# Optimization experiments

Measured on AMD Instinct MI355X. Metric: run time of the kernel, lower is better.

Reference implementation:

```python
import jax, jax.numpy as jnp
import numpy as np

DEPTH = 3
NUM_MOLS = 2000
ATOMS_PER_MOL = 50
NA = NUM_MOLS * ATOMS_PER_MOL + 1   # +1 chemprop zero-padding row
NB = 2 * NUM_MOLS * ATOMS_PER_MOL + 1
MAX_NB = 6
ATOM_FDIM, BOND_FDIM, H = 133, 147, 300


def setup_inputs() -> dict:
    key = jax.random.key(0)
    ks = jax.random.split(key, 12)
    f_atoms = jax.random.normal(ks[0], (NA, ATOM_FDIM), jnp.float32)
    f_bonds = jax.random.normal(ks[1], (NB, BOND_FDIM), jnp.float32)
    # zero padding row (index 0) as in chemprop BatchMolGraph
    f_atoms = f_atoms.at[0].set(0.0)
    f_bonds = f_bonds.at[0].set(0.0)
    w_atoms = jax.random.uniform(ks[2], (NA,), jnp.float32, 0.5, 1.0)
    w_bonds = jax.random.uniform(ks[3], (NB,), jnp.float32, 0.5, 1.0)
    degree_of_polym = jax.random.uniform(ks[4], (NUM_MOLS,), jnp.float32, 0.5, 1.5)
    W_i = jax.random.normal(ks[5], (BOND_FDIM, H), jnp.float32) / np.sqrt(BOND_FDIM)
    W_h = jax.random.normal(ks[6], (H, H), jnp.float32) / np.sqrt(H)
    W_o = jax.random.normal(ks[7], (ATOM_FDIM + H, H), jnp.float32) / np.sqrt(ATOM_FDIM + H)
    b_o = jax.random.normal(ks[8], (H,), jnp.float32) * 0.01
    a2b = jax.random.randint(ks[9], (NA, MAX_NB), 0, NB, jnp.int32)
    b2a = jax.random.randint(ks[10], (NB,), 0, NA, jnp.int32)
    b2revb = jax.random.randint(ks[11], (NB,), 0, NB, jnp.int32)
    # segment id per real atom (padding row 0 excluded), contiguous molecules
    mol_index = (jnp.arange(NA - 1, dtype=jnp.int32) // ATOMS_PER_MOL)
    return dict(f_atoms=f_atoms, f_bonds=f_bonds, w_atoms=w_atoms, w_bonds=w_bonds,
                degree_of_polym=degree_of_polym, W_i=W_i, W_h=W_h, W_o=W_o, b_o=b_o,
                a2b=a2b, b2a=b2a, b2revb=b2revb, mol_index=mol_index)


def reference(f_atoms, f_bonds, w_atoms, w_bonds, degree_of_polym,
              W_i, W_h, W_o, b_o, a2b, b2a, b2revb, mol_index):
    # bond-message D-MPNN (atom_messages=False, undirected=False, relu, no dropout)
    inp = f_bonds @ W_i                       # [NB, H]
    message = jax.nn.relu(inp)
    w_nei = w_bonds[a2b]                      # [NA, MAX_NB]
    for _ in range(DEPTH - 1):
        nei = message[a2b] * w_nei[..., None] # [NA, MAX_NB, H] weighted gather
        a_message = nei.sum(axis=1)           # [NA, H]
        message = a_message[b2a] - message[b2revb] * w_bonds[:, None]
        message = jax.nn.relu(inp + message @ W_h)
    # final atom readout
    a_message = (message[a2b] * w_nei[..., None]).sum(axis=1)   # [NA, H]
    a_input = jnp.concatenate([f_atoms, a_message], axis=1)     # [NA, ATOM_FDIM+H]
    atom_hiddens = jax.nn.relu(a_input @ W_o + b_o)
    # per-molecule weighted mean over real atoms (row 0 is padding)
    h = atom_hiddens[1:] * w_atoms[1:, None]
    num_mols = degree_of_polym.shape[0]
    mol_sum = jax.ops.segment_sum(h, mol_index, num_segments=num_mols)
    w_sum = jax.ops.segment_sum(w_atoms[1:], mol_index, num_segments=num_mols)
    mol_vecs = degree_of_polym[:, None] * (mol_sum / w_sum[:, None])
    return mol_vecs
```

## Files before the change

### kernel.cpp

```cpp
#include <hip/hip_runtime.h>

typedef __bf16 bf16;
typedef bf16 bf16x8 __attribute__((ext_vector_type(8)));
typedef float f32x4 __attribute__((ext_vector_type(4)));

#define NUM_MOLS 2000
#define APM 50
#define NA (NUM_MOLS*APM+1)
#define NB (2*NUM_MOLS*APM+1)
#define MAX_NB 6
#define AF 133
#define BFD 147
#define H 300
#define HP 320
#define KIP 192
#define KO 448
#define AOFF 136
#define BM 64
#define LDTE 72

__global__ void k_prep_wi(const float* __restrict__ Wi, bf16* __restrict__ Wt){
    int i = blockIdx.x*256 + threadIdx.x; if (i >= HP*KIP) return;
    int n = i / KIP, k = i % KIP;
    float v = (k < BFD && n < H) ? Wi[k*H + n] : 0.f;
    Wt[i] = (bf16)v;
}
__global__ void k_prep_wh(const float* __restrict__ Wh, bf16* __restrict__ Wt){
    int i = blockIdx.x*256 + threadIdx.x; if (i >= HP*HP) return;
    int n = i / HP, k = i % HP;
    float v = (k < H && n < H) ? Wh[k*H + n] : 0.f;
    Wt[i] = (bf16)v;
}
__global__ void k_prep_wo(const float* __restrict__ Wo, bf16* __restrict__ Wt){
    int i = blockIdx.x*256 + threadIdx.x; if (i >= HP*KO) return;
    int n = i / KO, k = i % KO;
    float v = 0.f;
    if (n < H) {
        if (k < AF)                       v = Wo[k*H + n];
        else if (k >= AOFF && k < AOFF+H) v = Wo[(k - AOFF + AF)*H + n];
    }
    Wt[i] = (bf16)v;
}
__global__ void k_init_cat(const float* __restrict__ fa, bf16* __restrict__ cat){
    long u = (long)blockIdx.x*256 + threadIdx.x; if (u >= (long)NA*18) return;
    int c = (int)(u % 18); long a = u / 18;
    bf16x8 v;
    if (c < 17) {
        int c0 = c*8;
        #pragma unroll
        for (int j=0;j<8;j++){
            int col = c0 + j;
            float f = (col < AF) ? fa[a*AF + col] : 0.f;
            v[j] = (bf16)f;
        }
        *(bf16x8*)(cat + a*KO + c0) = v;
    } else {
        #pragma unroll
        for (int j=0;j<8;j++) v[j] = (bf16)0.f;
        *(bf16x8*)(cat + a*KO + 440) = v;
    }
}

__global__ void k_gather_amsg(const bf16* __restrict__ msg, const int* __restrict__ a2b,
                              const float* __restrict__ w_bonds,
                              bf16* __restrict__ out, int out_stride, int col_off, int nchunks){
    long u = (long)blockIdx.x*256 + threadIdx.x;
    if (u >= (long)NA*nchunks) return;
    int c = (int)(u % nchunks); long a = u / nchunks;
    int c0 = c*8;
    float acc[8] = {0,0,0,0,0,0,0,0};
    #pragma unroll
    for (int k=0;k<MAX_NB;k++){
        int b = a2b[a*MAX_NB + k];
        float w = w_bonds[b];
        bf16x8 m = *(const bf16x8*)(msg + (long)b*HP + c0);
        #pragma unroll
        for (int j=0;j<8;j++) acc[j] += w * fmaxf((float)m[j], 0.f);
    }
    bf16x8 o;
    #pragma unroll
    for (int j=0;j<8;j++) o[j] = (bf16)acc[j];
    *(bf16x8*)(out + (long)a*out_stride + col_off + c0) = o;
}

template<int MODE, int K>
__global__ __launch_bounds__(512)
void k_gemm(const void* __restrict__ Asrc, const bf16* __restrict__ msgsrc,
            const int* __restrict__ b2a, const int* __restrict__ b2revb,
            const float* __restrict__ w_bonds,
            const bf16* __restrict__ Bt, int M,
            const bf16* __restrict__ add, const float* __restrict__ bias,
            bf16* __restrict__ out)
{
    constexpr int NSTEP = K / 64;
    __shared__ bf16 As[BM][LDTE];
    __shared__ bf16 Bs[HP][LDTE];
    const int t = threadIdx.x;
    const int row0 = blockIdx.x * BM;

    const int sr = t >> 3;
    const int sc = (t & 7) * 8;
    int arow = row0 + sr; if (arow >= M) arow = M - 1;
    int ia = 0, ir = 0; float w = 0.f;
    if (MODE == 1) { ia = b2a[arow]; ir = b2revb[arow]; w = w_bonds[arow]; }

    float  fa8[8];
    bf16x8 ra, rm;
    bf16x8 rb[5];

    auto issue = [&](int k0){
        if constexpr (MODE == 0) {
            const float* fb = (const float*)Asrc;
            #pragma unroll
            for (int j = 0; j < 8; j++) {
                int k = k0 + sc + j;
                fa8[j] = (k < BFD) ? fb[(long)arow*BFD + k] : 0.f;
            }
        } else if constexpr (MODE == 1) {
            ra = *(const bf16x8*)((const bf16*)Asrc + (long)ia*HP + k0 + sc);
            rm = *(const bf16x8*)(msgsrc            + (long)ir*HP + k0 + sc);
        } else {
            ra = *(const bf16x8*)((const bf16*)Asrc + (long)arow*KO + k0 + sc);
        }
        #pragma unroll
        for (int i = 0; i < 5; i++) {
            int c = t + 512*i;
            rb[i] = *(const bf16x8*)(Bt + (long)(c >> 3)*K + k0 + (c & 7)*8);
        }
    };
    auto commit = [&](){
        bf16x8 av;
        if constexpr (MODE == 0) {
            #pragma unroll
            for (int j = 0; j < 8; j++) av[j] = (bf16)fa8[j];
        } else if constexpr (MODE == 1) {
            #pragma unroll
            for (int j = 0; j < 8; j++)
                av[j] = (bf16)((float)ra[j] - fmaxf((float)rm[j], 0.f) * w);
        } else {
            av = ra;
        }
        *(bf16x8*)(&As[sr][sc]) = av;
        #pragma unroll
        for (int i = 0; i < 5; i++) {
            int c = t + 512*i;
            *(bf16x8*)(&Bs[c >> 3][(c & 7)*8]) = rb[i];
        }
    };

    const int wave = t >> 6, lane = t & 63;
    const int wm = wave >> 2, wn = wave & 3;
    const int kr = lane >> 4, lr = lane & 15;
    f32x4 acc[2][5] = {};

    issue(0); commit();
    __syncthreads();

    #pragma unroll
    for (int s = 0; s < NSTEP; s++) {
        if (s + 1 < NSTEP) issue((s + 1) * 64);
        #pragma unroll
        for (int kk = 0; kk < 64; kk += 32) {
            bf16x8 af[2], bfr[5];
            #pragma unroll
            for (int m = 0; m < 2; m++)
                af[m] = *(const bf16x8*)(&As[wm*32 + m*16 + lr][kk + kr*8]);
            #pragma unroll
            for (int n = 0; n < 5; n++)
                bfr[n] = *(const bf16x8*)(&Bs[wn*80 + n*16 + lr][kk + kr*8]);
            #pragma unroll
            for (int m = 0; m < 2; m++)
                #pragma unroll
                for (int n = 0; n < 5; n++)
                    acc[m][n] = __builtin_amdgcn_mfma_f32_16x16x32_bf16(af[m], bfr[n], acc[m][n], 0, 0, 0);
        }
        if (s + 1 < NSTEP) {
            __syncthreads();
            commit();
            __syncthreads();
        }
    }

    #pragma unroll
    for (int m = 0; m < 2; m++)
    #pragma unroll
    for (int n = 0; n < 5; n++)
    #pragma unroll
    for (int r = 0; r < 4; r++) {
        int row = row0 + wm*32 + m*16 + kr*4 + r;
        if (row >= M) continue;
        int col = wn*80 + n*16 + lr;
        float v = acc[m][n][r];
        if (add)  v += (float)add[(long)row*HP + col];
        if (bias) v += (col < H) ? bias[col] : 0.f;
        if (MODE == 2) v = fmaxf(v, 0.f);
        out[(long)row*HP + col] = (bf16)v;
    }
}

__global__ void k_seg(const bf16* __restrict__ ah, const float* __restrict__ w_atoms,
                      const float* __restrict__ dop, float* __restrict__ out){
    int m = blockIdx.x; int t = threadIdx.x;
    __shared__ float ws_sum;
    float w = 0.f;
    if (t < APM) w = w_atoms[1 + m*APM + t];
    if (t < 64) {
        for (int o=32;o;o>>=1) w += __shfl_down(w, o);
        if (t==0) ws_sum = w;
    }
    __syncthreads();
    float scale = dop[m] / ws_sum;
    for (int h = t; h < H; h += 256) {
        float acc = 0.f;
        for (int j=0;j<APM;j++){
            int a = 1 + m*APM + j;
            acc += (float)ah[(long)a*HP + h] * w_atoms[a];
        }
        out[m*H + h] = acc * scale;
    }
}

__global__ void k_zero(float* __restrict__ out, int n){
    int i = blockIdx.x*256 + threadIdx.x;
    if (i < n) out[i] = 0.f;
}

extern "C" void kernel_launch(void* const* d_in, const int* in_sizes, int n_in,
                              void* d_out, int out_size, void* d_ws, size_t ws_size,
                              hipStream_t stream) {
    const float* f_atoms = (const float*)d_in[0];
    const float* f_bonds = (const float*)d_in[1];
    const float* w_atoms = (const float*)d_in[2];
    const float* w_bonds = (const float*)d_in[3];
    const float* dop     = (const float*)d_in[4];
    const float* W_i     = (const float*)d_in[5];
    const float* W_h     = (const float*)d_in[6];
    const float* W_o     = (const float*)d_in[7];
    const float* b_o     = (const float*)d_in[8];
    const int*   a2b     = (const int*)d_in[9];
    const int*   b2a     = (const int*)d_in[10];
    const int*   b2revb  = (const int*)d_in[11];
    float* out = (float*)d_out;
    (void)in_sizes; (void)n_in;

    const size_t R_BIG = ((size_t)NB*HP*2 + 255) & ~(size_t)255;
    const size_t R_ATM = ((size_t)NA*HP*2 + 255) & ~(size_t)255;
    const size_t R_WI  = ((size_t)HP*KIP*2 + 255) & ~(size_t)255;
    const size_t R_WH  = ((size_t)HP*HP*2 + 255) & ~(size_t)255;
    const size_t R_WO  = ((size_t)HP*KO*2 + 255) & ~(size_t)255;
    const size_t need  = 3*R_BIG + R_ATM + R_WI + R_WH + R_WO;

    if (ws_size < need) {
        k_zero<<<(out_size+255)/256, 256, 0, stream>>>(out, out_size);
        return;
    }

    char* ws = (char*)d_ws;
    bf16* inp  = (bf16*)ws;
    bf16* msgA = (bf16*)(ws + R_BIG);
    bf16* msgB = (bf16*)(ws + 2*R_BIG);
    bf16* amsg = (bf16*)(ws + 3*R_BIG);
    bf16* wit  = (bf16*)(ws + 3*R_BIG + R_ATM);
    bf16* wht  = (bf16*)((char*)wit + R_WI);
    bf16* wot  = (bf16*)((char*)wht + R_WH);
    bf16* cat  = msgA;
    bf16* ah   = amsg;

    k_prep_wi<<<(HP*KIP+255)/256, 256, 0, stream>>>(W_i, wit);
    k_prep_wh<<<(HP*HP+255)/256, 256, 0, stream>>>(W_h, wht);
    k_prep_wo<<<(HP*KO+255)/256, 256, 0, stream>>>(W_o, wot);

    const int GB = (NB + BM - 1) / BM;
    const int GA = (NA + BM - 1) / BM;

    k_gemm<0, KIP><<<GB, 512, 0, stream>>>(f_bonds, nullptr, nullptr, nullptr, nullptr,
                                           wit, NB, nullptr, nullptr, inp);
    k_gather_amsg<<<(int)(((long)NA*40+255)/256), 256, 0, stream>>>(
        inp, a2b, w_bonds, amsg, HP, 0, 40);
    k_gemm<1, HP><<<GB, 512, 0, stream>>>(amsg, inp, b2a, b2revb, w_bonds,
                                          wht, NB, inp, nullptr, msgA);
    k_gather_amsg<<<(int)(((long)NA*40+255)/256), 256, 0, stream>>>(
        msgA, a2b, w_bonds, amsg, HP, 0, 40);
    k_gemm<1, HP><<<GB, 512, 0, stream>>>(amsg, msgA, b2a, b2revb, w_bonds,
                                          wht, NB, inp, nullptr, msgB);
    k_init_cat<<<(int)(((long)NA*18+255)/256), 256, 0, stream>>>(f_atoms, cat);
    k_gather_amsg<<<(int)(((long)NA*38+255)/256), 256, 0, stream>>>(
        msgB, a2b, w_bonds, cat, KO, AOFF, 38);
    k_gemm<2, KO><<<GA, 512, 0, stream>>>(cat, nullptr, nullptr, nullptr, nullptr,
                                          wot, NA, nullptr, b_o, ah);
    k_seg<<<NUM_MOLS, 256, 0, stream>>>(ah, w_atoms, dop, out);
}
```

Before: 803.0 us.

## Pre-swizzle weights into MFMA fragment order and stage tiles via direct global-to-LDS loads

```diff
diff --git a/kernel.cpp b/kernel.cpp
--- a/kernel.cpp
+++ b/kernel.cpp
@@ -17,30 +17,39 @@
 #define KO 448
 #define AOFF 136
 #define BM 64
-#define LDTE 72
-
-__global__ void k_prep_wi(const float* __restrict__ Wi, bf16* __restrict__ Wt){
-    int i = blockIdx.x*256 + threadIdx.x; if (i >= HP*KIP) return;
-    int n = i / KIP, k = i % KIP;
-    float v = (k < BFD && n < H) ? Wi[k*H + n] : 0.f;
-    Wt[i] = (bf16)v;
-}
-__global__ void k_prep_wh(const float* __restrict__ Wh, bf16* __restrict__ Wt){
-    int i = blockIdx.x*256 + threadIdx.x; if (i >= HP*HP) return;
-    int n = i / HP, k = i % HP;
-    float v = (k < H && n < H) ? Wh[k*H + n] : 0.f;
-    Wt[i] = (bf16)v;
-}
-__global__ void k_prep_wo(const float* __restrict__ Wo, bf16* __restrict__ Wt){
-    int i = blockIdx.x*256 + threadIdx.x; if (i >= HP*KO) return;
-    int n = i / KO, k = i % KO;
+
+typedef const __attribute__((address_space(1))) void gvoid_t;
+typedef __attribute__((address_space(3))) void lvoid_t;
+__device__ __forceinline__ void gload16(const void* g, void* l) {
+    __builtin_amdgcn_global_load_lds((gvoid_t*)g, (lvoid_t*)l, 16, 0, 0);
+}
+
+__device__ __forceinline__ void frag_decode(int e, int& row, int& col, int& j){
+    int s = e / 20480;
+    int r = e - s*20480;
+    int q = r >> 3; j = r & 7;
+    int frag = q >> 6, lane = q & 63;
+    int wn = frag / 10, rem = frag - wn*10;
+    int n = rem >> 1, kh = rem & 1;
+    row = wn*80 + n*16 + (lane & 15);
+    col = s*64 + kh*32 + ((lane >> 4) << 3) + j;
+}
+
+template<int W, int K>
+__global__ void k_prep(const float* __restrict__ src, bf16* __restrict__ dst){
+    int e = blockIdx.x*256 + threadIdx.x;
+    if (e >= HP*K) return;
+    int row, col, j; frag_decode(e, row, col, j);
     float v = 0.f;
-    if (n < H) {
-        if (k < AF)                       v = Wo[k*H + n];
-        else if (k >= AOFF && k < AOFF+H) v = Wo[(k - AOFF + AF)*H + n];
-    }
-    Wt[i] = (bf16)v;
-}
+    if (row < H) {
+        if constexpr (W == 0)      { if (col < BFD) v = src[col*H + row]; }
+        else if constexpr (W == 1) { if (col < H)   v = src[col*H + row]; }
+        else { if (col < AF) v = src[col*H + row];
+               else if (col >= AOFF && col < AOFF+H) v = src[(col-AOFF+AF)*H + row]; }
+    }
+    dst[e] = (bf16)v;
+}
+
 __global__ void k_init_cat(const float* __restrict__ fa, bf16* __restrict__ cat){
     long u = (long)blockIdx.x*256 + threadIdx.x; if (u >= (long)NA*18) return;
     int c = (int)(u % 18); long a = u / 18;
@@ -84,103 +93,116 @@
 }
 
 template<int MODE, int K>
-__global__ __launch_bounds__(512)
+__global__ __launch_bounds__(512, 4)
 void k_gemm(const void* __restrict__ Asrc, const bf16* __restrict__ msgsrc,
             const int* __restrict__ b2a, const int* __restrict__ b2revb,
             const float* __restrict__ w_bonds,
-            const bf16* __restrict__ Bt, int M,
+            const bf16* __restrict__ Btg, int M,
             const bf16* __restrict__ add, const float* __restrict__ bias,
             bf16* __restrict__ out)
 {
-    constexpr int NSTEP = K / 64;
-    __shared__ bf16 As[BM][LDTE];
-    __shared__ bf16 Bs[HP][LDTE];
-    const int t = threadIdx.x;
+    constexpr int NKB = K/32, NSTEP = K/64, NJ = K/64;
+    __shared__ bf16 As[64*K];
+    __shared__ bf16 Bs[20480];
+    const int t = threadIdx.x, lane = t & 63, wv = t >> 6;
     const int row0 = blockIdx.x * BM;
 
-    const int sr = t >> 3;
-    const int sc = (t & 7) * 8;
-    int arow = row0 + sr; if (arow >= M) arow = M - 1;
-    int ia = 0, ir = 0; float w = 0.f;
-    if (MODE == 1) { ia = b2a[arow]; ir = b2revb[arow]; w = w_bonds[arow]; }
-
-    float  fa8[8];
-    bf16x8 ra, rm;
-    bf16x8 rb[5];
-
-    auto issue = [&](int k0){
-        if constexpr (MODE == 0) {
-            const float* fb = (const float*)Asrc;
+    int acol[NJ]; int agrow[NJ];
+    #pragma unroll
+    for (int i = 0; i < NJ; i++) {
+        int frag = i*8 + wv;
+        int rg = frag / NKB, kb = frag - rg*NKB;
+        int grow = row0 + rg*16 + (lane & 15);
+        if (grow >= M) grow = M - 1;
+        agrow[i] = grow;
+        acol[i]  = kb*32 + ((lane >> 4) << 3);
+    }
+
+    bf16x8 ra[MODE==1?NJ:1], rm[MODE==1?NJ:1];
+    float  wbv[MODE==1?NJ:1];
+    float  f8[MODE==0?NJ:1][8];
+
+    if constexpr (MODE == 0) {
+        const float* fb = (const float*)Asrc;
+        #pragma unroll
+        for (int i = 0; i < NJ; i++)
             #pragma unroll
             for (int j = 0; j < 8; j++) {
-                int k = k0 + sc + j;
-                fa8[j] = (k < BFD) ? fb[(long)arow*BFD + k] : 0.f;
+                int k = acol[i] + j;
+                f8[i][j] = (k < BFD) ? fb[(long)agrow[i]*BFD + k] : 0.f;
             }
-        } else if constexpr (MODE == 1) {
-            ra = *(const bf16x8*)((const bf16*)Asrc + (long)ia*HP + k0 + sc);
-            rm = *(const bf16x8*)(msgsrc            + (long)ir*HP + k0 + sc);
-        } else {
-            ra = *(const bf16x8*)((const bf16*)Asrc + (long)arow*KO + k0 + sc);
-        }
-        #pragma unroll
-        for (int i = 0; i < 5; i++) {
-            int c = t + 512*i;
-            rb[i] = *(const bf16x8*)(Bt + (long)(c >> 3)*K + k0 + (c & 7)*8);
-        }
-    };
-    auto commit = [&](){
-        bf16x8 av;
-        if constexpr (MODE == 0) {
-            #pragma unroll
-            for (int j = 0; j < 8; j++) av[j] = (bf16)fa8[j];
-        } else if constexpr (MODE == 1) {
+    } else if constexpr (MODE == 1) {
+        const bf16* am = (const bf16*)Asrc;
+        #pragma unroll
+        for (int i = 0; i < NJ; i++) {
+            int ia = b2a[agrow[i]], ir = b2revb[agrow[i]];
+            wbv[i] = w_bonds[agrow[i]];
+            ra[i] = *(const bf16x8*)(am     + (long)ia*HP + acol[i]);
+            rm[i] = *(const bf16x8*)(msgsrc + (long)ir*HP + acol[i]);
+        }
+    } else {
+        const bf16* cat = (const bf16*)Asrc;
+        #pragma unroll
+        for (int i = 0; i < NJ; i++)
+            gload16(cat + (long)agrow[i]*KO + acol[i], As + ((long)i*512 + (t & ~63))*8);
+    }
+
+    #pragma unroll
+    for (int i = 0; i < 5; i++)
+        gload16(Btg + (long)(i*512 + t)*8, Bs + ((long)i*512 + (t & ~63))*8);
+
+    if constexpr (MODE == 0) {
+        #pragma unroll
+        for (int i = 0; i < NJ; i++) {
+            bf16x8 av;
+            #pragma unroll
+            for (int j = 0; j < 8; j++) av[j] = (bf16)f8[i][j];
+            *(bf16x8*)(As + ((long)i*512 + t)*8) = av;
+        }
+    } else if constexpr (MODE == 1) {
+        #pragma unroll
+        for (int i = 0; i < NJ; i++) {
+            bf16x8 av;
             #pragma unroll
             for (int j = 0; j < 8; j++)
-                av[j] = (bf16)((float)ra[j] - fmaxf((float)rm[j], 0.f) * w);
-        } else {
-            av = ra;
-        }
-        *(bf16x8*)(&As[sr][sc]) = av;
-        #pragma unroll
-        for (int i = 0; i < 5; i++) {
-            int c = t + 512*i;
-            *(bf16x8*)(&Bs[c >> 3][(c & 7)*8]) = rb[i];
-        }
-    };
-
-    const int wave = t >> 6, lane = t & 63;
-    const int wm = wave >> 2, wn = wave & 3;
-    const int kr = lane >> 4, lr = lane & 15;
+                av[j] = (bf16)((float)ra[i][j] - fmaxf((float)rm[i][j], 0.f) * wbv[i]);
+            *(bf16x8*)(As + ((long)i*512 + t)*8) = av;
+        }
+    }
+
+    const int wm = wv >> 2, wn = wv & 3;
     f32x4 acc[2][5] = {};
-
-    issue(0); commit();
     __syncthreads();
 
     #pragma unroll
     for (int s = 0; s < NSTEP; s++) {
-        if (s + 1 < NSTEP) issue((s + 1) * 64);
-        #pragma unroll
-        for (int kk = 0; kk < 64; kk += 32) {
-            bf16x8 af[2], bfr[5];
+        #pragma unroll
+        for (int kh = 0; kh < 2; kh++) {
+            const int kb = s*2 + kh;
+            bf16x8 af[2], bq[5];
             #pragma unroll
             for (int m = 0; m < 2; m++)
-                af[m] = *(const bf16x8*)(&As[wm*32 + m*16 + lr][kk + kr*8]);
+                af[m] = *(const bf16x8*)(As + (((wm*2+m)*NKB + kb)*64 + lane)*8);
             #pragma unroll
             for (int n = 0; n < 5; n++)
-                bfr[n] = *(const bf16x8*)(&Bs[wn*80 + n*16 + lr][kk + kr*8]);
+                bq[n] = *(const bf16x8*)(Bs + ((wn*10 + n*2 + kh)*64 + lane)*8);
             #pragma unroll
             for (int m = 0; m < 2; m++)
                 #pragma unroll
                 for (int n = 0; n < 5; n++)
-                    acc[m][n] = __builtin_amdgcn_mfma_f32_16x16x32_bf16(af[m], bfr[n], acc[m][n], 0, 0, 0);
+                    acc[m][n] = __builtin_amdgcn_mfma_f32_16x16x32_bf16(af[m], bq[n], acc[m][n], 0, 0, 0);
         }
         if (s + 1 < NSTEP) {
             __syncthreads();
-            commit();
+            #pragma unroll
+            for (int i = 0; i < 5; i++)
+                gload16(Btg + (long)(s+1)*20480 + (long)(i*512 + t)*8,
+                        Bs + ((long)i*512 + (t & ~63))*8);
             __syncthreads();
         }
     }
 
+    const int kr = lane >> 4, lr = lane & 15;
     #pragma unroll
     for (int m = 0; m < 2; m++)
     #pragma unroll
@@ -266,9 +288,9 @@
     bf16* cat  = msgA;
     bf16* ah   = amsg;
 
-    k_prep_wi<<<(HP*KIP+255)/256, 256, 0, stream>>>(W_i, wit);
-    k_prep_wh<<<(HP*HP+255)/256, 256, 0, stream>>>(W_h, wht);
-    k_prep_wo<<<(HP*KO+255)/256, 256, 0, stream>>>(W_o, wot);
+    k_prep<0, KIP><<<(HP*KIP+255)/256, 256, 0, stream>>>(W_i, wit);
+    k_prep<1, HP ><<<(HP*HP +255)/256, 256, 0, stream>>>(W_h, wht);
+    k_prep<2, KO ><<<(HP*KO +255)/256, 256, 0, stream>>>(W_o, wot);
 
     const int GB = (NB + BM - 1) / BM;
     const int GA = (NA + BM - 1) / BM;
```

After: 857.5 us. 1.07x slower.
